# Kernel tuning notes

Hardware: AMD Instinct MI355X
Metric: run time of the kernel (lower is better)

The kernel has to match this reference:

```python
import jax, jax.numpy as jnp
import numpy as np

B, S, D_IN, D_OUT = 4, 2048, 4096, 4096


def setup_inputs() -> dict:
    key = jax.random.key(0)
    k_x, k_w, k_s, k_z, k_b = jax.random.split(key, 5)
    x = jax.random.normal(k_x, (B, S, D_IN), dtype=jnp.float32)
    # int8 weight codes stored as int32 (values in [-128, 127])
    weight = jax.random.randint(k_w, (D_OUT, D_IN), -128, 128, dtype=jnp.int32)
    # per-output-channel quantization params
    scale = jax.random.uniform(k_s, (D_OUT, 1), dtype=jnp.float32, minval=0.005, maxval=0.02)
    zero_point = jax.random.uniform(k_z, (D_OUT, 1), dtype=jnp.float32, minval=-2.0, maxval=2.0)
    bias = jax.random.normal(k_b, (D_OUT,), dtype=jnp.float32)
    return {"x": x, "weight": weight, "scale": scale, "zero_point": zero_point, "bias": bias}


def reference(x, weight, scale, zero_point, bias):
    # Dequantize: w_fp = (int8_codes - zero_point) * scale  -> [D_OUT, D_IN]
    w_fp = (weight.astype(jnp.float32) - zero_point) * scale
    # F.linear: out = x @ w_fp.T + bias
    out = jnp.einsum("bsi,oi->bso", x, w_fp) + bias
    return out
```

## Files before the change

kernel.cpp:

```cpp
#include <hip/hip_runtime.h>
#include <hip/hip_bf16.h>

typedef int  i32x4 __attribute__((ext_vector_type(4)));

__global__ __launch_bounds__(256) void prep_x_i8(const float* __restrict__ x,
                                                 int* __restrict__ xq,
                                                 float* __restrict__ rsum,
                                                 float* __restrict__ rscale,
                                                 int K) {
    const int row = blockIdx.x;
    const float* xr = x + (size_t)row * K;
    __shared__ float xs[4096];
    float mx = 0.f;
    for (int c = threadIdx.x * 4; c < K; c += blockDim.x * 4) {
        float4 v = *reinterpret_cast<const float4*>(xr + c);
        *reinterpret_cast<float4*>(xs + c) = v;
        mx = fmaxf(mx, fmaxf(fmaxf(fabsf(v.x), fabsf(v.y)),
                             fmaxf(fabsf(v.z), fabsf(v.w))));
    }
    #pragma unroll
    for (int off = 32; off > 0; off >>= 1) mx = fmaxf(mx, __shfl_down(mx, off));
    __shared__ float wmax[4];
    __shared__ float s_sx, s_inv;
    const int lane = threadIdx.x & 63, wv = threadIdx.x >> 6;
    if (lane == 0) wmax[wv] = mx;
    __syncthreads();
    if (threadIdx.x == 0) {
        float m = fmaxf(fmaxf(wmax[0], wmax[1]), fmaxf(wmax[2], wmax[3]));
        m = fmaxf(m, 1e-20f);
        s_sx = m / 127.f; s_inv = 127.f / m;
    }
    __syncthreads();
    const float inv = s_inv;
    int qs = 0;
    for (int c = threadIdx.x * 4; c < K; c += blockDim.x * 4) {
        float4 v = *reinterpret_cast<const float4*>(xs + c);
        const int q0 = __float2int_rn(v.x * inv), q1 = __float2int_rn(v.y * inv);
        const int q2 = __float2int_rn(v.z * inv), q3 = __float2int_rn(v.w * inv);
        qs += q0 + q1 + q2 + q3;
        const unsigned p = (unsigned)(q0 & 255) | ((unsigned)(q1 & 255) << 8) |
                           ((unsigned)(q2 & 255) << 16) | ((unsigned)(q3 & 255) << 24);
        xq[((size_t)row * K + c) >> 2] = (int)p;
    }
    #pragma unroll
    for (int off = 32; off > 0; off >>= 1) qs += __shfl_down(qs, off);
    __shared__ int wqs[4];
    if (lane == 0) wqs[wv] = qs;
    __syncthreads();
    if (threadIdx.x == 0) {
        const int t = wqs[0] + wqs[1] + wqs[2] + wqs[3];
        rsum[row] = s_sx * (float)t;
        rscale[row] = s_sx;
    }
}

__global__ __launch_bounds__(256) void prep_w_i8(const int* __restrict__ w,
                                                 int* __restrict__ wq) {
    const size_t i = (size_t)blockIdx.x * blockDim.x + threadIdx.x;
    const int4* src = reinterpret_cast<const int4*>(w) + i * 4;
    int4 a = src[0], b = src[1], c = src[2], d = src[3];
    int4 o;
    o.x = (a.x & 255) | ((a.y & 255) << 8) | ((a.z & 255) << 16) | ((a.w & 255) << 24);
    o.y = (b.x & 255) | ((b.y & 255) << 8) | ((b.z & 255) << 16) | ((b.w & 255) << 24);
    o.z = (c.x & 255) | ((c.y & 255) << 8) | ((c.z & 255) << 16) | ((c.w & 255) << 24);
    o.w = (d.x & 255) | ((d.y & 255) << 8) | ((d.z & 255) << 16) | ((d.w & 255) << 24);
    reinterpret_cast<int4*>(wq)[i] = o;
}

__device__ __forceinline__ void async16(void* lds, const void* g) {
    __builtin_amdgcn_global_load_lds(
        (const __attribute__((address_space(1))) unsigned*)g,
        (__attribute__((address_space(3))) unsigned*)lds, 16, 0, 0);
}

__global__ __launch_bounds__(512, 2) void qgemm8i(
    const char* __restrict__ A, const char* __restrict__ B,
    const float* __restrict__ rsum, const float* __restrict__ rscale,
    const float* __restrict__ scale, const float* __restrict__ zp,
    const float* __restrict__ bias, float* __restrict__ C,
    int M, int N, int K) {
    extern __shared__ char smem[];
    char* const AsB = smem;
    char* const BsB = smem + 65536;

    const int tid  = threadIdx.x;
    const int lane = tid & 63;
    const int wid  = tid >> 6;
    const int wm = wid >> 2, wn = wid & 3;
    const int l15 = lane & 15;

    const int nbn = N >> 8;
    int wg = blockIdx.x;
    wg = (wg & 7) * (gridDim.x >> 3) + (wg >> 3);
    const int bm = wg / nbn, bn = wg % nbn;

    const int r0s = tid >> 2, sls = tid & 3;
    size_t a_src[2], b_src[2];
    int lds_off[2];
    #pragma unroll
    for (int j = 0; j < 2; ++j) {
        const int row = r0s + j * 128;
        const int sl  = sls ^ ((row >> 1) & 3);
        a_src[j] = ((size_t)(bm * 256 + row)) * K + sl * 16;
        b_src[j] = ((size_t)(bn * 256 + row)) * K + sl * 16;
        lds_off[j] = (j * 512 + tid) * 16;
    }

    auto stageA = [&](int u, int ks, int buf) {
        const int kc = u * 128 + ks * 64;
        char* const dst = AsB + (buf * 2 + ks) * 16384;
        #pragma unroll
        for (int j = 0; j < 2; ++j) async16(dst + lds_off[j], A + a_src[j] + kc);
    };
    auto stageB = [&](int u, int ks, int buf) {
        const int kc = u * 128 + ks * 64;
        char* const dst = BsB + (buf * 2 + ks) * 16384;
        #pragma unroll
        for (int j = 0; j < 2; ++j) async16(dst + lds_off[j], B + b_src[j] + kc);
    };

    const int sw16 = (((lane >> 4) ^ ((lane >> 1) & 3)) << 4);
    const int a_ro = (wm * 128 + l15) * 64 + sw16;
    const int b_ro = (wn * 64 + l15) * 64 + sw16;

    i32x4 acc[8][4] = {};
    i32x4 af0[4], af1[4], bfr0[4], bfr1[4];

    const int NT  = K >> 7;
    const int NIT = NT >> 1;

#define READ_AF(DST, BUF, KS, QM)                                              \
    {                                                                          \
        const char* _ha = AsB + ((BUF) * 2 + (KS)) * 16384;                    \
        _Pragma("unroll")                                                      \
        for (int m = 0; m < 4; ++m)                                            \
            DST[m] = *(const i32x4*)(_ha + a_ro + ((QM) * 4 + m) * 1024);      \
    }

#define READ_BF(DST, BUF, KS)                                                  \
    {                                                                          \
        const char* _hb = BsB + ((BUF) * 2 + (KS)) * 16384;                    \
        _Pragma("unroll")                                                      \
        for (int n = 0; n < 4; ++n)                                            \
            DST[n] = *(const i32x4*)(_hb + b_ro + n * 1024);                   \
    }

#define MFMA16(QM, AF, BF)                                                     \
    __builtin_amdgcn_s_setprio(1);                                             \
    _Pragma("unroll")                                                          \
    for (int m = 0; m < 4; ++m)                                                \
        _Pragma("unroll")                                                      \
        for (int n = 0; n < 4; ++n)                                            \
            acc[(QM) * 4 + m][n] = __builtin_amdgcn_mfma_i32_16x16x64_i8(      \
                AF[m], BF[n], acc[(QM) * 4 + m][n], 0, 0, 0);                  \
    __builtin_amdgcn_s_setprio(0);

#define LGKM(N) asm volatile("s_waitcnt lgkmcnt(" #N ")" ::: "memory");        \
                __builtin_amdgcn_sched_barrier(0);
#define ENDPH   __builtin_amdgcn_sched_barrier(0);                             \
                asm volatile("s_barrier" ::: "memory");
#define VM8     asm volatile("s_waitcnt vmcnt(8)" ::: "memory");

    stageB(0, 0, 0); stageA(0, 0, 0); stageB(0, 1, 0); stageA(0, 1, 0);
    asm volatile("s_waitcnt vmcnt(4)" ::: "memory");
    stageB(1, 0, 1); stageA(1, 0, 1); stageB(1, 1, 1);
    asm volatile("s_waitcnt vmcnt(6)" ::: "memory");
    asm volatile("s_barrier" ::: "memory");
    READ_AF(af1, 0, 0, 0);
    READ_BF(bfr0, 0, 0);

    #pragma unroll 1
    for (int i = 0; i < NIT; ++i) {
        const int t  = 2 * i;
        const int u1 = t + 1;
        int u2 = t + 2; if (u2 >= NT) u2 = NT - 1;
        int u3 = t + 3; if (u3 >= NT) u3 = NT - 1;

        READ_AF(af0, 0, 0, 1);
        stageA(u1, 1, 1);
        LGKM(4)
        MFMA16(0, af1, bfr0);
        ENDPH
        VM8
        READ_AF(af1, 0, 1, 0);
        READ_BF(bfr1, 0, 1);
        stageB(u2, 0, 0);
        LGKM(8)
        MFMA16(1, af0, bfr0);
        ENDPH
        READ_AF(af0, 0, 1, 1);
        stageA(u2, 0, 0);
        LGKM(4)
        MFMA16(0, af1, bfr1);
        ENDPH
        VM8
        READ_AF(af1, 1, 0, 0);
        READ_BF(bfr0, 1, 0);
        stageB(u2, 1, 0);
        LGKM(8)
        MFMA16(1, af0, bfr1);
        ENDPH
        READ_AF(af0, 1, 0, 1);
        stageA(u2, 1, 0);
        LGKM(4)
        MFMA16(0, af1, bfr0);
        ENDPH
        VM8
        READ_AF(af1, 1, 1, 0);
        READ_BF(bfr1, 1, 1);
        stageB(u3, 0, 1);
        LGKM(8)
        MFMA16(1, af0, bfr0);
        ENDPH
        READ_AF(af0, 1, 1, 1);
        stageA(u3, 0, 1);
        LGKM(4)
        MFMA16(0, af1, bfr1);
        ENDPH
        VM8
        READ_AF(af1, 0, 0, 0);
        READ_BF(bfr0, 0, 0);
        stageB(u3, 1, 1);
        LGKM(8)
        MFMA16(1, af0, bfr1);
        ENDPH
    }
#undef READ_AF
#undef READ_BF
#undef MFMA16
#undef LGKM
#undef ENDPH
#undef VM8

    float sc[4], zz[4], bb[4];
    #pragma unroll
    for (int n = 0; n < 4; ++n) {
        const int o = bn * 256 + wn * 64 + n * 16 + l15;
        sc[n] = scale[o]; zz[n] = zp[o]; bb[n] = bias[o];
    }
    const int hi4 = (lane >> 4) << 2;
    #pragma unroll
    for (int mf = 0; mf < 8; ++mf) {
        const int r0 = bm * 256 + wm * 128 + mf * 16 + hi4;
        float rs[4], sx[4];
        #pragma unroll
        for (int i = 0; i < 4; ++i) { rs[i] = rsum[r0 + i]; sx[i] = rscale[r0 + i]; }
        #pragma unroll
        for (int n = 0; n < 4; ++n) {
            const int o = bn * 256 + wn * 64 + n * 16 + l15;
            #pragma unroll
            for (int i = 0; i < 4; ++i)
                C[(size_t)(r0 + i) * N + o] =
                    sc[n] * (sx[i] * (float)acc[mf][n][i] - zz[n] * rs[i]) + bb[n];
        }
    }
}

extern "C" void kernel_launch(void* const* d_in, const int* in_sizes, int n_in,
                              void* d_out, int out_size, void* d_ws, size_t ws_size,
                              hipStream_t stream) {
    const float* x     = (const float*)d_in[0];
    const int*   w     = (const int*)d_in[1];
    const float* scale = (const float*)d_in[2];
    const float* zp    = (const float*)d_in[3];
    const float* bias  = (const float*)d_in[4];
    float* out = (float*)d_out;

    const int N = in_sizes[2];
    const int K = in_sizes[1] / N;
    const int M = in_sizes[0] / K;

    char*  xq  = (char*)d_ws;
    char*  wq  = (char*)d_ws + (size_t)M * K;
    float* rs  = (float*)((char*)d_ws + (size_t)M * K + (size_t)N * K);
    float* rsc = rs + M;

    prep_x_i8<<<M, 256, 0, stream>>>(x, (int*)xq, rs, rsc, K);
    prep_w_i8<<<(int)(((size_t)N * K / 16) / 256), 256, 0, stream>>>(w, (int*)wq);

    (void)hipFuncSetAttribute((const void*)qgemm8i,
                              hipFuncAttributeMaxDynamicSharedMemorySize, 131072);
    const int nwg = (M / 256) * (N / 256);
    qgemm8i<<<nwg, 512, 131072, stream>>>(xq, wq, rs, rsc, scale, zp, bias,
                                          out, M, N, K);
}
```

Measured before the change: 181.8 us.

## Shrink int8 GEMM tile to 128x128 with 4-stage LDS ring pipeline

Replaces the 256x256-tile, 8-wave int8 MFMA GEMM with a 128x128-tile, 4-wave kernel. Each wave now holds a 64x64 accumulator, and LDS is reorganised into a 4-slot ring of 64-wide K slices with a simpler two-phase prefetch schedule. The aim is more workgroups per CU and a simpler pipeline. In exchange, data reuse per tile drops by half, which raises global and LDS traffic per MFMA.

```diff
diff --git a/kernel.cpp b/kernel.cpp
--- a/kernel.cpp
+++ b/kernel.cpp
@@ -73,23 +73,23 @@
         (__attribute__((address_space(3))) unsigned*)lds, 16, 0, 0);
 }
 
-__global__ __launch_bounds__(512, 2) void qgemm8i(
+__global__ __launch_bounds__(256, 2) void qgemm4i(
     const char* __restrict__ A, const char* __restrict__ B,
     const float* __restrict__ rsum, const float* __restrict__ rscale,
     const float* __restrict__ scale, const float* __restrict__ zp,
     const float* __restrict__ bias, float* __restrict__ C,
     int M, int N, int K) {
     extern __shared__ char smem[];
-    char* const AsB = smem;
-    char* const BsB = smem + 65536;
+    char* const AsR = smem;
+    char* const BsR = smem + 32768;
 
     const int tid  = threadIdx.x;
     const int lane = tid & 63;
     const int wid  = tid >> 6;
-    const int wm = wid >> 2, wn = wid & 3;
+    const int wm = wid >> 1, wn = wid & 1;
     const int l15 = lane & 15;
 
-    const int nbn = N >> 8;
+    const int nbn = N >> 7;
     int wg = blockIdx.x;
     wg = (wg & 7) * (gridDim.x >> 3) + (wg >> 3);
     const int bm = wg / nbn, bn = wg % nbn;
@@ -99,155 +99,109 @@
     int lds_off[2];
     #pragma unroll
     for (int j = 0; j < 2; ++j) {
-        const int row = r0s + j * 128;
+        const int row = r0s + j * 64;
         const int sl  = sls ^ ((row >> 1) & 3);
-        a_src[j] = ((size_t)(bm * 256 + row)) * K + sl * 16;
-        b_src[j] = ((size_t)(bn * 256 + row)) * K + sl * 16;
-        lds_off[j] = (j * 512 + tid) * 16;
-    }
-
-    auto stageA = [&](int u, int ks, int buf) {
-        const int kc = u * 128 + ks * 64;
-        char* const dst = AsB + (buf * 2 + ks) * 16384;
-        #pragma unroll
-        for (int j = 0; j < 2; ++j) async16(dst + lds_off[j], A + a_src[j] + kc);
+        a_src[j] = ((size_t)(bm * 128 + row)) * K + sl * 16;
+        b_src[j] = ((size_t)(bn * 128 + row)) * K + sl * 16;
+        lds_off[j] = (j * 256 + tid) * 16;
+    }
+
+    auto STAGE = [&](int u, int sl) {
+        const int kc = u * 64;
+        char* const da = AsR + sl * 8192;
+        char* const db = BsR + sl * 8192;
+        #pragma unroll
+        for (int j = 0; j < 2; ++j) async16(da + lds_off[j], A + a_src[j] + kc);
+        #pragma unroll
+        for (int j = 0; j < 2; ++j) async16(db + lds_off[j], B + b_src[j] + kc);
     };
-    auto stageB = [&](int u, int ks, int buf) {
-        const int kc = u * 128 + ks * 64;
-        char* const dst = BsB + (buf * 2 + ks) * 16384;
-        #pragma unroll
-        for (int j = 0; j < 2; ++j) async16(dst + lds_off[j], B + b_src[j] + kc);
-    };
 
     const int sw16 = (((lane >> 4) ^ ((lane >> 1) & 3)) << 4);
-    const int a_ro = (wm * 128 + l15) * 64 + sw16;
+    const int a_ro = (wm * 64 + l15) * 64 + sw16;
     const int b_ro = (wn * 64 + l15) * 64 + sw16;
 
-    i32x4 acc[8][4] = {};
-    i32x4 af0[4], af1[4], bfr0[4], bfr1[4];
-
-    const int NT  = K >> 7;
-    const int NIT = NT >> 1;
-
-#define READ_AF(DST, BUF, KS, QM)                                              \
+    i32x4 acc[4][4] = {};
+    i32x4 afA[4], bfA[4], afB[4], bfB[4];
+
+#define READF(AF, BF, SL)                                                      \
     {                                                                          \
-        const char* _ha = AsB + ((BUF) * 2 + (KS)) * 16384;                    \
+        const char* _ha = AsR + (SL) * 8192;                                   \
+        const char* _hb = BsR + (SL) * 8192;                                   \
         _Pragma("unroll")                                                      \
         for (int m = 0; m < 4; ++m)                                            \
-            DST[m] = *(const i32x4*)(_ha + a_ro + ((QM) * 4 + m) * 1024);      \
-    }
-
-#define READ_BF(DST, BUF, KS)                                                  \
-    {                                                                          \
-        const char* _hb = BsB + ((BUF) * 2 + (KS)) * 16384;                    \
+            AF[m] = *(const i32x4*)(_ha + a_ro + m * 1024);                    \
         _Pragma("unroll")                                                      \
         for (int n = 0; n < 4; ++n)                                            \
-            DST[n] = *(const i32x4*)(_hb + b_ro + n * 1024);                   \
-    }
-
-#define MFMA16(QM, AF, BF)                                                     \
+            BF[n] = *(const i32x4*)(_hb + b_ro + n * 1024);                    \
+    }
+
+#define MFMA16(AF, BF)                                                         \
     __builtin_amdgcn_s_setprio(1);                                             \
     _Pragma("unroll")                                                          \
     for (int m = 0; m < 4; ++m)                                                \
         _Pragma("unroll")                                                      \
         for (int n = 0; n < 4; ++n)                                            \
-            acc[(QM) * 4 + m][n] = __builtin_amdgcn_mfma_i32_16x16x64_i8(      \
-                AF[m], BF[n], acc[(QM) * 4 + m][n], 0, 0, 0);                  \
+            acc[m][n] = __builtin_amdgcn_mfma_i32_16x16x64_i8(                 \
+                AF[m], BF[n], acc[m][n], 0, 0, 0);                             \
     __builtin_amdgcn_s_setprio(0);
 
-#define LGKM(N) asm volatile("s_waitcnt lgkmcnt(" #N ")" ::: "memory");        \
-                __builtin_amdgcn_sched_barrier(0);
-#define ENDPH   __builtin_amdgcn_sched_barrier(0);                             \
-                asm volatile("s_barrier" ::: "memory");
-#define VM8     asm volatile("s_waitcnt vmcnt(8)" ::: "memory");
-
-    stageB(0, 0, 0); stageA(0, 0, 0); stageB(0, 1, 0); stageA(0, 1, 0);
+#define LGKM8  asm volatile("s_waitcnt lgkmcnt(8)" ::: "memory");              \
+               __builtin_amdgcn_sched_barrier(0);
+#define VM4    asm volatile("s_waitcnt vmcnt(4)" ::: "memory");
+#define ENDPH  __builtin_amdgcn_sched_barrier(0);                              \
+               asm volatile("s_barrier" ::: "memory");
+
+    const int NS = K >> 6;
+
+    STAGE(0, 0); STAGE(1, 1); STAGE(2, 2);
     asm volatile("s_waitcnt vmcnt(4)" ::: "memory");
-    stageB(1, 0, 1); stageA(1, 0, 1); stageB(1, 1, 1);
-    asm volatile("s_waitcnt vmcnt(6)" ::: "memory");
     asm volatile("s_barrier" ::: "memory");
-    READ_AF(af1, 0, 0, 0);
-    READ_BF(bfr0, 0, 0);
+    READF(afA, bfA, 0);
 
     #pragma unroll 1
-    for (int i = 0; i < NIT; ++i) {
-        const int t  = 2 * i;
-        const int u1 = t + 1;
-        int u2 = t + 2; if (u2 >= NT) u2 = NT - 1;
-        int u3 = t + 3; if (u3 >= NT) u3 = NT - 1;
-
-        READ_AF(af0, 0, 0, 1);
-        stageA(u1, 1, 1);
-        LGKM(4)
-        MFMA16(0, af1, bfr0);
-        ENDPH
-        VM8
-        READ_AF(af1, 0, 1, 0);
-        READ_BF(bfr1, 0, 1);
-        stageB(u2, 0, 0);
-        LGKM(8)
-        MFMA16(1, af0, bfr0);
-        ENDPH
-        READ_AF(af0, 0, 1, 1);
-        stageA(u2, 0, 0);
-        LGKM(4)
-        MFMA16(0, af1, bfr1);
-        ENDPH
-        VM8
-        READ_AF(af1, 1, 0, 0);
-        READ_BF(bfr0, 1, 0);
-        stageB(u2, 1, 0);
-        LGKM(8)
-        MFMA16(1, af0, bfr1);
-        ENDPH
-        READ_AF(af0, 1, 0, 1);
-        stageA(u2, 1, 0);
-        LGKM(4)
-        MFMA16(0, af1, bfr0);
-        ENDPH
-        VM8
-        READ_AF(af1, 1, 1, 0);
-        READ_BF(bfr1, 1, 1);
-        stageB(u3, 0, 1);
-        LGKM(8)
-        MFMA16(1, af0, bfr0);
-        ENDPH
-        READ_AF(af0, 1, 1, 1);
-        stageA(u3, 0, 1);
-        LGKM(4)
-        MFMA16(0, af1, bfr1);
-        ENDPH
-        VM8
-        READ_AF(af1, 0, 0, 0);
-        READ_BF(bfr0, 0, 0);
-        stageB(u3, 1, 1);
-        LGKM(8)
-        MFMA16(1, af0, bfr1);
-        ENDPH
-    }
-#undef READ_AF
-#undef READ_BF
+    for (int i = 0; i < NS / 2; ++i) {
+        const int s = 2 * i;
+        {
+            READF(afB, bfB, (s + 1) & 3);
+            int u = s + 3; if (u >= NS) u = NS - 1;
+            STAGE(u, (s + 3) & 3);
+            LGKM8
+            MFMA16(afA, bfA);
+            VM4
+            ENDPH
+        }
+        {
+            READF(afA, bfA, (s + 2) & 3);
+            int u = s + 4; if (u >= NS) u = NS - 1;
+            STAGE(u, (s + 4) & 3);
+            LGKM8
+            MFMA16(afB, bfB);
+            VM4
+            ENDPH
+        }
+    }
+#undef READF
 #undef MFMA16
-#undef LGKM
+#undef LGKM8
+#undef VM4
 #undef ENDPH
-#undef VM8
 
     float sc[4], zz[4], bb[4];
     #pragma unroll
     for (int n = 0; n < 4; ++n) {
-        const int o = bn * 256 + wn * 64 + n * 16 + l15;
+        const int o = bn * 128 + wn * 64 + n * 16 + l15;
         sc[n] = scale[o]; zz[n] = zp[o]; bb[n] = bias[o];
     }
     const int hi4 = (lane >> 4) << 2;
     #pragma unroll
-    for (int mf = 0; mf < 8; ++mf) {
-        const int r0 = bm * 256 + wm * 128 + mf * 16 + hi4;
+    for (int mf = 0; mf < 4; ++mf) {
+        const int r0 = bm * 128 + wm * 64 + mf * 16 + hi4;
         float rs[4], sx[4];
         #pragma unroll
         for (int i = 0; i < 4; ++i) { rs[i] = rsum[r0 + i]; sx[i] = rscale[r0 + i]; }
         #pragma unroll
         for (int n = 0; n < 4; ++n) {
-            const int o = bn * 256 + wn * 64 + n * 16 + l15;
+            const int o = bn * 128 + wn * 64 + n * 16 + l15;
             #pragma unroll
             for (int i = 0; i < 4; ++i)
                 C[(size_t)(r0 + i) * N + o] =
@@ -278,9 +232,9 @@
     prep_x_i8<<<M, 256, 0, stream>>>(x, (int*)xq, rs, rsc, K);
     prep_w_i8<<<(int)(((size_t)N * K / 16) / 256), 256, 0, stream>>>(w, (int*)wq);
 
-    (void)hipFuncSetAttribute((const void*)qgemm8i,
-                              hipFuncAttributeMaxDynamicSharedMemorySize, 131072);
-    const int nwg = (M / 256) * (N / 256);
-    qgemm8i<<<nwg, 512, 131072, stream>>>(xq, wq, rs, rsc, scale, zp, bias,
-                                          out, M, N, K);
-}
+    (void)hipFuncSetAttribute((const void*)qgemm4i,
+                              hipFuncAttributeMaxDynamicSharedMemorySize, 65536);
+    const int nwg = (M / 128) * (N / 128);
+    qgemm4i<<<nwg, 256, 65536, stream>>>(xq, wq, rs, rsc, scale, zp, bias,
+                                         out, M, N, K);
+}
```

New measurement: 242.6 us. +33.4%, slower.
